# Kernel optimization log

Hardware: AMD Instinct MI355X
Metric: run time of the kernel (lower is better)

The kernel has to match this reference:

```python
import jax, jax.numpy as jnp
import numpy as np

BS, Q, NC, T, NI = 16, 1000, 80, 100, 8
IMG_W, IMG_H = 1333.0, 800.0
ALPHA, GAMMA = 0.25, 2.0
W_CLASS, W_BBOX, W_GIOU = 2.0, 5.0, 2.0


def _rand_boxes(key, n):
    k1, k2 = jax.random.split(key)
    cxcy = jax.random.uniform(k1, (n, 2)) * jnp.array([IMG_W, IMG_H])
    wh = jax.random.uniform(k2, (n, 2)) * 300.0 + 8.0
    return jnp.concatenate([cxcy - wh / 2, cxcy + wh / 2], axis=-1).astype(jnp.float32)


def setup_inputs() -> dict:
    key = jax.random.key(0)
    k1, k2, k3, k4, k5 = jax.random.split(key, 5)
    img_sz = jnp.array([IMG_W, IMG_H, IMG_W, IMG_H], jnp.float32)
    return {
        'pred_logits': jax.random.normal(k1, (BS, Q, NC), jnp.float32),
        'pred_boxes': _rand_boxes(k2, BS * Q).reshape(BS, Q, 4),
        'tgt_bbox': _rand_boxes(k3, BS * T),
        'ign_bbox': _rand_boxes(k4, BS * NI),
        'image_size_xyxy': jnp.tile(img_sz, (BS, 1)),
        'image_size_xyxy_tgt': jnp.tile(img_sz, (BS * T, 1)),
        'tgt_ids': jax.random.randint(k5, (BS * T,), 0, NC),
    }


def _area(b):
    return (b[:, 2] - b[:, 0]) * (b[:, 3] - b[:, 1])


def _pairwise_inter(b1, b2):
    # b1: [N,4], b2: [M,4] -> inter area [N,M]
    lt = jnp.maximum(b1[:, None, :2], b2[None, :, :2])
    rb = jnp.minimum(b1[:, None, 2:], b2[None, :, 2:])
    wh = jnp.clip(rb - lt, 0.0)
    return wh[..., 0] * wh[..., 1]


def _giou(b1, b2):
    inter = _pairwise_inter(b1, b2)
    union = _area(b1)[:, None] + _area(b2)[None, :] - inter
    iou = inter / union
    # smallest enclosing box
    lt = jnp.minimum(b1[:, None, :2], b2[None, :, :2])
    rb = jnp.maximum(b1[:, None, 2:], b2[None, :, 2:])
    wh = jnp.clip(rb - lt, 0.0)
    enc = wh[..., 0] * wh[..., 1]
    return iou - (enc - union) / enc


def reference(pred_logits, pred_boxes, tgt_bbox, ign_bbox, image_size_xyxy,
              image_size_xyxy_tgt, tgt_ids):
    bs, q, nc = pred_logits.shape
    n = bs * q
    out_prob = jax.nn.sigmoid(pred_logits.reshape(n, nc))          # focal branch
    out_bbox = pred_boxes.reshape(n, 4)

    # focal classification cost, gathered at target labels
    p = out_prob[:, tgt_ids]                                       # [N, T_total]
    neg = (1 - ALPHA) * p ** GAMMA * (-jnp.log(1 - p + 1e-8))
    pos = ALPHA * (1 - p) ** GAMMA * (-jnp.log(p + 1e-8))
    cost_class = pos - neg

    # L1 cost on normalized boxes
    img_out = jnp.repeat(image_size_xyxy, q, axis=0)               # [N,4]
    ob = out_bbox / img_out
    tb = tgt_bbox / image_size_xyxy_tgt
    cost_bbox = jnp.abs(ob[:, None, :] - tb[None, :, :]).sum(-1)   # [N, T_total]

    cost_giou = -_giou(out_bbox, tgt_bbox)

    # IoA of predictions vs ignore boxes (intersection / pred area)
    ioa = _pairwise_inter(out_bbox, ign_bbox) / _area(out_bbox)[:, None]

    C = W_BBOX * cost_bbox + W_CLASS * cost_class + W_GIOU * cost_giou

    # per-image block-diagonal extraction (homogeneous T, NI per image)
    t = tgt_bbox.shape[0] // bs
    ni = ign_bbox.shape[0] // bs
    idx = jnp.arange(bs)
    C_diag = C.reshape(bs, q, bs, t)[idx, :, idx, :]               # [bs, Q, T]
    ioa_diag = ioa.reshape(bs, q, bs, ni)[idx, :, idx, :]          # [bs, Q, NI]
    return C_diag, ioa_diag
```

## Files before the change

kernel.cpp:

```cpp
#include <hip/hip_runtime.h>

#define BS 16
#define Q  1000
#define NC 80
#define T  100
#define NI 8

#define ALPHA   0.25f
#define W_CLASS 2.0f
#define W_BBOX  5.0f
#define W_GIOU  2.0f

__global__ __launch_bounds__(128) void matcher_kernel(
    const float* __restrict__ pred_logits,
    const float* __restrict__ pred_boxes,
    const float* __restrict__ tgt_bbox,
    const float* __restrict__ ign_bbox,
    const float* __restrict__ img_sz,
    const float* __restrict__ img_sz_tgt,
    const int*   __restrict__ tgt_ids,
    float* __restrict__ out)
{
    const int n   = blockIdx.x;
    const int b   = n / Q;
    const int tid = threadIdx.x;

    const float4 pb  = *(const float4*)(pred_boxes + (size_t)n * 4);
    const float4 isz = *(const float4*)(img_sz     + (size_t)b * 4);
    const float area_p = (pb.z - pb.x) * (pb.w - pb.y);
    const float obx = pb.x / isz.x;
    const float oby = pb.y / isz.y;
    const float obz = pb.z / isz.z;
    const float obw = pb.w / isz.w;

    if (tid < T) {
        const int j = tid;
        const int r = b * T + j;
        const float4 tb  = *(const float4*)(tgt_bbox   + (size_t)r * 4);
        const float4 tsz = *(const float4*)(img_sz_tgt + (size_t)r * 4);

        const float cb = fabsf(obx - tb.x / tsz.x)
                       + fabsf(oby - tb.y / tsz.y)
                       + fabsf(obz - tb.z / tsz.z)
                       + fabsf(obw - tb.w / tsz.w);

        const int   cls   = tgt_ids[r];
        const float logit = pred_logits[(size_t)n * NC + cls];
        const float p     = 1.0f / (1.0f + expf(-logit));
        const float pos   =  ALPHA        * (1.0f - p) * (1.0f - p) * (-logf(p + 1e-8f));
        const float neg   = (1.0f - ALPHA) * p * p                   * (-logf(1.0f - p + 1e-8f));
        const float cost_class = pos - neg;

        const float ltx = fmaxf(pb.x, tb.x), lty = fmaxf(pb.y, tb.y);
        const float rbx = fminf(pb.z, tb.z), rby = fminf(pb.w, tb.w);
        const float iw  = fmaxf(rbx - ltx, 0.0f), ih = fmaxf(rby - lty, 0.0f);
        const float inter = iw * ih;
        const float area_t = (tb.z - tb.x) * (tb.w - tb.y);
        const float uni  = area_p + area_t - inter;
        const float iou  = inter / uni;
        const float eltx = fminf(pb.x, tb.x), elty = fminf(pb.y, tb.y);
        const float erbx = fmaxf(pb.z, tb.z), erby = fmaxf(pb.w, tb.w);
        const float ew   = fmaxf(erbx - eltx, 0.0f), eh = fmaxf(erby - elty, 0.0f);
        const float enc  = ew * eh;
        const float giou = iou - (enc - uni) / enc;

        out[(size_t)n * T + j] = W_BBOX * cb + W_CLASS * cost_class + W_GIOU * (-giou);
    } else if (tid < T + NI) {
        const int j = tid - T;
        const int r = b * NI + j;
        const float4 ib = *(const float4*)(ign_bbox + (size_t)r * 4);
        const float ltx = fmaxf(pb.x, ib.x), lty = fmaxf(pb.y, ib.y);
        const float rbx = fminf(pb.z, ib.z), rby = fminf(pb.w, ib.w);
        const float iw  = fmaxf(rbx - ltx, 0.0f), ih = fmaxf(rby - lty, 0.0f);
        const float inter = iw * ih;
        out[(size_t)BS * Q * T + (size_t)n * NI + j] = inter / area_p;
    }
}

extern "C" void kernel_launch(void* const* d_in, const int* in_sizes, int n_in,
                              void* d_out, int out_size, void* d_ws, size_t ws_size,
                              hipStream_t stream) {
    const float* pred_logits = (const float*)d_in[0];
    const float* pred_boxes  = (const float*)d_in[1];
    const float* tgt_bbox    = (const float*)d_in[2];
    const float* ign_bbox    = (const float*)d_in[3];
    const float* img_sz      = (const float*)d_in[4];
    const float* img_sz_tgt  = (const float*)d_in[5];
    const int*   tgt_ids     = (const int*)d_in[6];
    float* out = (float*)d_out;

    matcher_kernel<<<BS * Q, 128, 0, stream>>>(
        pred_logits, pred_boxes, tgt_bbox, ign_bbox, img_sz, img_sz_tgt, tgt_ids, out);
}
```

Before: 80.09 us.

## Flatten to one thread per output element and use fast rcp/exp2/log intrinsics

Replaces the one-block-per-prediction mapping, where 128 threads are launched but only 108 do work, with a flat grid of 256-thread blocks that covers every output element, cost and IoA alike. This removes idle lanes and the per-block launch granularity. Divisions, exp and log are swapped for AMDGCN hardware rcp, exp2 and log intrinsics to cut instruction latency. In exchange each thread reloads the prediction box and image size instead of sharing them, uses integer division to recover indices, and the approximate intrinsics may change numerics slightly.

```diff
diff --git a/kernel.cpp b/kernel.cpp
--- a/kernel.cpp
+++ b/kernel.cpp
@@ -1,17 +1,22 @@
 #include <hip/hip_runtime.h>
 
-#define BS 16
-#define Q  1000
-#define NC 80
-#define T  100
-#define NI 8
+constexpr int BS = 16, Q = 1000, NC = 80, T = 100, NI = 8;
+constexpr int CTOT = BS * Q * T;
+constexpr int ITOT = BS * Q * NI;
+constexpr int TOT  = CTOT + ITOT;
 
 #define ALPHA   0.25f
 #define W_CLASS 2.0f
 #define W_BBOX  5.0f
 #define W_GIOU  2.0f
 
-__global__ __launch_bounds__(128) void matcher_kernel(
+__device__ __forceinline__ float rcp(float x)  { return __builtin_amdgcn_rcpf(x); }
+__device__ __forceinline__ float ex2(float x)  { return __builtin_amdgcn_exp2f(x); }
+__device__ __forceinline__ float lg2(float x)  { return __builtin_amdgcn_logf(x); }
+#define LOG2E 1.44269504088896f
+#define LN2   0.69314718055995f
+
+__global__ __launch_bounds__(256) void matcher_kernel(
     const float* __restrict__ pred_logits,
     const float* __restrict__ pred_boxes,
     const float* __restrict__ tgt_bbox,
@@ -21,59 +26,58 @@
     const int*   __restrict__ tgt_ids,
     float* __restrict__ out)
 {
-    const int n   = blockIdx.x;
-    const int b   = n / Q;
-    const int tid = threadIdx.x;
+    const int idx = blockIdx.x * 256 + threadIdx.x;
+    if (idx >= TOT) return;
 
-    const float4 pb  = *(const float4*)(pred_boxes + (size_t)n * 4);
-    const float4 isz = *(const float4*)(img_sz     + (size_t)b * 4);
-    const float area_p = (pb.z - pb.x) * (pb.w - pb.y);
-    const float obx = pb.x / isz.x;
-    const float oby = pb.y / isz.y;
-    const float obz = pb.z / isz.z;
-    const float obw = pb.w / isz.w;
+    if (idx < CTOT) {
+        const int n = idx / T;
+        const int j = idx - n * T;
+        const int b = n / Q;
+        const int r = b * T + j;
 
-    if (tid < T) {
-        const int j = tid;
-        const int r = b * T + j;
-        const float4 tb  = *(const float4*)(tgt_bbox   + (size_t)r * 4);
-        const float4 tsz = *(const float4*)(img_sz_tgt + (size_t)r * 4);
+        const float4 pb  = *(const float4*)(pred_boxes  + (size_t)n * 4);
+        const float4 tb  = *(const float4*)(tgt_bbox    + (size_t)r * 4);
+        const float4 isz = *(const float4*)(img_sz      + (size_t)b * 4);
+        const float4 tsz = *(const float4*)(img_sz_tgt  + (size_t)r * 4);
 
-        const float cb = fabsf(obx - tb.x / tsz.x)
-                       + fabsf(oby - tb.y / tsz.y)
-                       + fabsf(obz - tb.z / tsz.z)
-                       + fabsf(obw - tb.w / tsz.w);
+        const float cb = fabsf(pb.x * rcp(isz.x) - tb.x * rcp(tsz.x))
+                       + fabsf(pb.y * rcp(isz.y) - tb.y * rcp(tsz.y))
+                       + fabsf(pb.z * rcp(isz.z) - tb.z * rcp(tsz.z))
+                       + fabsf(pb.w * rcp(isz.w) - tb.w * rcp(tsz.w));
 
         const int   cls   = tgt_ids[r];
         const float logit = pred_logits[(size_t)n * NC + cls];
-        const float p     = 1.0f / (1.0f + expf(-logit));
-        const float pos   =  ALPHA        * (1.0f - p) * (1.0f - p) * (-logf(p + 1e-8f));
-        const float neg   = (1.0f - ALPHA) * p * p                   * (-logf(1.0f - p + 1e-8f));
+        const float p     = rcp(1.0f + ex2(-logit * LOG2E));
+        const float omp   = 1.0f - p;
+        const float pos   =  ALPHA         * omp * omp * (-(lg2(p   + 1e-8f) * LN2));
+        const float neg   = (1.0f - ALPHA) * p   * p   * (-(lg2(omp + 1e-8f) * LN2));
         const float cost_class = pos - neg;
 
-        const float ltx = fmaxf(pb.x, tb.x), lty = fmaxf(pb.y, tb.y);
-        const float rbx = fminf(pb.z, tb.z), rby = fminf(pb.w, tb.w);
-        const float iw  = fmaxf(rbx - ltx, 0.0f), ih = fmaxf(rby - lty, 0.0f);
+        const float area_p = (pb.z - pb.x) * (pb.w - pb.y);
+        const float area_t = (tb.z - tb.x) * (tb.w - tb.y);
+        const float iw  = fmaxf(fminf(pb.z, tb.z) - fmaxf(pb.x, tb.x), 0.0f);
+        const float ih  = fmaxf(fminf(pb.w, tb.w) - fmaxf(pb.y, tb.y), 0.0f);
         const float inter = iw * ih;
-        const float area_t = (tb.z - tb.x) * (tb.w - tb.y);
-        const float uni  = area_p + area_t - inter;
-        const float iou  = inter / uni;
-        const float eltx = fminf(pb.x, tb.x), elty = fminf(pb.y, tb.y);
-        const float erbx = fmaxf(pb.z, tb.z), erby = fmaxf(pb.w, tb.w);
-        const float ew   = fmaxf(erbx - eltx, 0.0f), eh = fmaxf(erby - elty, 0.0f);
-        const float enc  = ew * eh;
-        const float giou = iou - (enc - uni) / enc;
+        const float uni   = area_p + area_t - inter;
+        const float ew  = fmaxf(fmaxf(pb.z, tb.z) - fminf(pb.x, tb.x), 0.0f);
+        const float eh  = fmaxf(fmaxf(pb.w, tb.w) - fminf(pb.y, tb.y), 0.0f);
+        const float enc = ew * eh;
+        const float giou = inter * rcp(uni) - (enc - uni) * rcp(enc);
 
-        out[(size_t)n * T + j] = W_BBOX * cb + W_CLASS * cost_class + W_GIOU * (-giou);
-    } else if (tid < T + NI) {
-        const int j = tid - T;
+        out[idx] = W_BBOX * cb + W_CLASS * cost_class - W_GIOU * giou;
+    } else {
+        const int k = idx - CTOT;
+        const int n = k >> 3;
+        const int j = k & (NI - 1);
+        const int b = n / Q;
         const int r = b * NI + j;
-        const float4 ib = *(const float4*)(ign_bbox + (size_t)r * 4);
-        const float ltx = fmaxf(pb.x, ib.x), lty = fmaxf(pb.y, ib.y);
-        const float rbx = fminf(pb.z, ib.z), rby = fminf(pb.w, ib.w);
-        const float iw  = fmaxf(rbx - ltx, 0.0f), ih = fmaxf(rby - lty, 0.0f);
-        const float inter = iw * ih;
-        out[(size_t)BS * Q * T + (size_t)n * NI + j] = inter / area_p;
+
+        const float4 pb = *(const float4*)(pred_boxes + (size_t)n * 4);
+        const float4 ib = *(const float4*)(ign_bbox   + (size_t)r * 4);
+        const float area_p = (pb.z - pb.x) * (pb.w - pb.y);
+        const float iw  = fmaxf(fminf(pb.z, ib.z) - fmaxf(pb.x, ib.x), 0.0f);
+        const float ih  = fmaxf(fminf(pb.w, ib.w) - fmaxf(pb.y, ib.y), 0.0f);
+        out[idx] = iw * ih * rcp(area_p);
     }
 }
 
@@ -89,6 +93,7 @@
     const int*   tgt_ids     = (const int*)d_in[6];
     float* out = (float*)d_out;
 
-    matcher_kernel<<<BS * Q, 128, 0, stream>>>(
+    const int blocks = (TOT + 255) / 256;
+    matcher_kernel<<<blocks, 256, 0, stream>>>(
         pred_logits, pred_boxes, tgt_bbox, ign_bbox, img_sz, img_sz_tgt, tgt_ids, out);
 }
```

Result: faster. 73.49 us (-8.2%).
